# Kernel tuning notes

Measured on AMD Instinct MI355X. Metric: run time of the kernel, lower is better.

Reference implementation:

```python
import jax, jax.numpy as jnp
import numpy as np

D_MODEL = 2048
N_HEADS = 16
D_HEAD = 128
D_LATENT = 512


def setup_inputs() -> dict:
    key = jax.random.key(0)
    ks = jax.random.split(key, 5)
    s = lambda fan_in: 1.0 / np.sqrt(fan_in)
    x = jax.random.normal(ks[0], (2, 2048, D_MODEL), dtype=jnp.float32)
    # nn.Linear weights stored as [out, in]; we keep [in, out] for x @ W
    W_q = jax.random.uniform(ks[1], (D_MODEL, N_HEADS * D_HEAD), jnp.float32, -s(D_MODEL), s(D_MODEL))
    W_kv_down = jax.random.uniform(ks[2], (D_MODEL, D_LATENT), jnp.float32, -s(D_MODEL), s(D_MODEL))
    W_kv_up = jax.random.uniform(ks[3], (D_LATENT, N_HEADS * D_HEAD), jnp.float32, -s(D_LATENT), s(D_LATENT))
    W_o = jax.random.uniform(ks[4], (N_HEADS * D_HEAD, D_MODEL), jnp.float32, -s(N_HEADS * D_HEAD), s(N_HEADS * D_HEAD))
    return {"x": x, "W_q": W_q, "W_kv_down": W_kv_down, "W_kv_up": W_kv_up, "W_o": W_o}


def reference(x, W_q, W_kv_down, W_kv_up, W_o):
    B, S, _ = x.shape
    # q: [B, H, S, Dh]
    q = (x @ W_q).reshape(B, S, N_HEADS, D_HEAD).transpose(0, 2, 1, 3)
    # latent compression then up-projection; shared K = V
    latent = x @ W_kv_down                      # [B, S, Dl]
    kv = (latent @ W_kv_up).reshape(B, S, N_HEADS, D_HEAD).transpose(0, 2, 1, 3)
    scale = 1.0 / np.sqrt(D_HEAD).astype(np.float32)
    scores = jnp.einsum('bhqd,bhkd->bhqk', q, kv) * scale  # [B,H,S,S]
    probs = jax.nn.softmax(scores, axis=-1)
    out = jnp.einsum('bhqk,bhkd->bhqd', probs, kv)          # [B,H,S,Dh]
    out = out.transpose(0, 2, 1, 3).reshape(B, S, N_HEADS * D_HEAD)
    return out @ W_o
```

## Files before the change

### kernel.cpp

```cpp
#include <hip/hip_runtime.h>

typedef __attribute__((ext_vector_type(8))) __bf16 bf16x8;
typedef __attribute__((ext_vector_type(4))) float f32x4;
typedef __attribute__((ext_vector_type(8))) unsigned short u16x8;
typedef __attribute__((ext_vector_type(4))) unsigned short u16x4;

#define MFMA16(a, b, c) __builtin_amdgcn_mfma_f32_16x16x32_bf16((a), (b), (c), 0, 0, 0)

__device__ __forceinline__ unsigned short f2bf(float f) {
    unsigned int u = __float_as_uint(f);
    unsigned int r = (u + 0x7FFFu + ((u >> 16) & 1u)) >> 16;
    return (unsigned short)r;
}

__device__ __forceinline__ void transpose_tile(const float* __restrict__ in,
                                               unsigned short* __restrict__ out,
                                               int R, int C, int bx, int by) {
    __shared__ float tile[32][33];
    const int tx = threadIdx.x & 31, ty = threadIdx.x >> 5;
    const int c0 = bx * 32, r0 = by * 32;
#pragma unroll
    for (int i = 0; i < 4; ++i)
        tile[ty + i * 8][tx] = in[(size_t)(r0 + ty + i * 8) * C + c0 + tx];
    __syncthreads();
#pragma unroll
    for (int i = 0; i < 4; ++i)
        out[(size_t)(c0 + ty + i * 8) * R + r0 + tx] = f2bf(tile[tx][ty + i * 8]);
}

__global__ __launch_bounds__(256) void k_prep(const float* __restrict__ x,
                                              const float* __restrict__ Wq,
                                              const float* __restrict__ Wkvd,
                                              const float* __restrict__ Wkvu,
                                              const float* __restrict__ Wo,
                                              unsigned short* __restrict__ xb,
                                              unsigned short* __restrict__ Wcat_t,
                                              unsigned short* __restrict__ Wkvu_t,
                                              unsigned short* __restrict__ Wo_t) {
    const int i = blockIdx.x;
    if (i < 8192) {
        const int idx = i * 256 + threadIdx.x;
        const float4 v = ((const float4*)x)[idx];
        u16x4 o = { f2bf(v.x), f2bf(v.y), f2bf(v.z), f2bf(v.w) };
        ((u16x4*)xb)[idx] = o;
    } else if (i < 12288) {
        const int j = i - 8192;
        transpose_tile(Wq, Wcat_t, 2048, 2048, j & 63, j >> 6);
    } else if (i < 13312) {
        const int j = i - 12288;
        transpose_tile(Wkvd, Wcat_t + 2048 * 2048, 2048, 512, j & 15, j >> 4);
    } else if (i < 14336) {
        const int j = i - 13312;
        transpose_tile(Wkvu, Wkvu_t, 512, 2048, j & 63, j >> 6);
    } else {
        const int j = i - 14336;
        transpose_tile(Wo, Wo_t, 2048, 2048, j & 63, j >> 6);
    }
}

template <int OUT_MODE>
__global__ __launch_bounds__(256) void k_gemm_bt(const unsigned short* __restrict__ A,
                                                 const unsigned short* __restrict__ B,
                                                 void* __restrict__ Cv,
                                                 unsigned short* __restrict__ Ct,
                                                 int M, int N, int K, float alpha) {
    __shared__ alignas(16) unsigned short As[2 * 128 * 32];
    __shared__ alignas(16) unsigned short Bs[2 * 128 * 32];
    const int tid = threadIdx.x;
    const int wave = tid >> 6;
    const int lane = tid & 63;
    const int l16 = lane & 15;
    const int quad = lane >> 4;
    const int bm = blockIdx.x * 128;
    const int bn = blockIdx.y * 128;
    const int wm = (wave >> 1) * 64;
    const int wn = (wave & 1) * 64;

    const f32x4 fzero = {0.f, 0.f, 0.f, 0.f};
    f32x4 acc[4][4];
#pragma unroll
    for (int i = 0; i < 4; ++i)
#pragma unroll
        for (int j = 0; j < 4; ++j) acc[i][j] = fzero;

    auto AsL = (__attribute__((address_space(3))) unsigned short*)As;
    auto BsL = (__attribute__((address_space(3))) unsigned short*)Bs;

    const int c0 = wave * 128 + lane;

    auto stage = [&](int kt32) {
        const int boff = (kt32 & 1) * (128 * 32);
        const int kt = kt32 * 32;
#pragma unroll
        for (int j = 0; j < 2; ++j) {
            const int c = c0 + j * 64;
            __builtin_amdgcn_global_load_lds(
                (const __attribute__((address_space(1))) void*)(A + (size_t)(bm + (c >> 2)) * K + kt + (c & 3) * 8),
                (__attribute__((address_space(3))) void*)(AsL + boff + c * 8), 16, 0, 0);
            __builtin_amdgcn_global_load_lds(
                (const __attribute__((address_space(1))) void*)(B + (size_t)(bn + (c >> 2)) * K + kt + (c & 3) * 8),
                (__attribute__((address_space(3))) void*)(BsL + boff + c * 8), 16, 0, 0);
        }
    };

    const int nk = K >> 5;
    stage(0);
    for (int kt32 = 0; kt32 < nk; ++kt32) {
        __syncthreads();
        if (kt32 + 1 < nk) stage(kt32 + 1);
        const unsigned short* Ab = As + (kt32 & 1) * (128 * 32);
        const unsigned short* Bb = Bs + (kt32 & 1) * (128 * 32);

        bf16x8 af[4], bfr[4];
#pragma unroll
        for (int mt = 0; mt < 4; ++mt)
            af[mt] = *(const bf16x8*)(Ab + (wm + mt * 16 + l16) * 32 + quad * 8);
#pragma unroll
        for (int nt = 0; nt < 4; ++nt)
            bfr[nt] = *(const bf16x8*)(Bb + (wn + nt * 16 + l16) * 32 + quad * 8);
#pragma unroll
        for (int mt = 0; mt < 4; ++mt)
#pragma unroll
            for (int nt = 0; nt < 4; ++nt)
                acc[mt][nt] = MFMA16(af[mt], bfr[nt], acc[mt][nt]);
    }

#pragma unroll
    for (int mt = 0; mt < 4; ++mt)
#pragma unroll
        for (int nt = 0; nt < 4; ++nt) {
            const int row0 = bm + wm + mt * 16 + quad * 4;
            const int col = bn + wn + nt * 16 + l16;
            u16x4 pk;
#pragma unroll
            for (int r = 0; r < 4; ++r) {
                const float v0 = acc[mt][nt][r];
                if (OUT_MODE == 0) {
                    ((float*)Cv)[(size_t)(row0 + r) * N + col] = v0 * alpha;
                } else if (OUT_MODE == 3) {
                    if (col < 2048)
                        ((unsigned short*)Cv)[(size_t)(row0 + r) * 2048 + col] = f2bf(v0 * alpha);
                    else
                        Ct[(size_t)(row0 + r) * 512 + (col - 2048)] = f2bf(v0);
                } else {
                    const unsigned short b = f2bf(v0 * alpha);
                    ((unsigned short*)Cv)[(size_t)(row0 + r) * N + col] = b;
                    pk[r] = b;
                }
            }
            if (OUT_MODE == 2) {
                const size_t ti =
                    ((size_t)((row0 >> 11) * (N >> 7) + (col >> 7)) * 128 + (col & 127)) * 2048 +
                    (row0 & 2047);
                *(u16x4*)(Ct + ti) = pk;
            }
        }
}

__global__ __launch_bounds__(256, 2) void k_attn(const unsigned short* __restrict__ Q,
                                                 const unsigned short* __restrict__ KV,
                                                 const unsigned short* __restrict__ KVT,
                                                 unsigned short* __restrict__ O) {
    __shared__ alignas(16) unsigned short Ks[2 * 64 * 128];
    __shared__ alignas(16) unsigned short Vt[2 * 128 * 64];
    __shared__ alignas(16) unsigned short Ps[4 * 32 * 64];

    const int tid = threadIdx.x;
    const int wave = tid >> 6, lane = tid & 63;
    const int l16 = lane & 15, quad = lane >> 4;
    const int l8 = l16 & 7;
    const int qt = blockIdx.x;
    const int bh = blockIdx.y;
    const size_t tokbase = (size_t)(bh >> 4) * 2048;
    const int hcol = (bh & 15) * 128;
    const unsigned short* kvt_head = KVT + (size_t)bh * (128 * 2048);

    bf16x8 qf[2][4];
    const int qrow0 = qt * 128 + wave * 32;
#pragma unroll
    for (int nt = 0; nt < 2; ++nt) {
        const unsigned short* qp =
            Q + (tokbase + qrow0 + nt * 16 + l16) * 2048 + hcol + quad * 8;
#pragma unroll
        for (int kd = 0; kd < 4; ++kd) qf[nt][kd] = *(const bf16x8*)(qp + kd * 32);
    }

    const f32x4 fzero = {0.f, 0.f, 0.f, 0.f};
    f32x4 o_acc[8][2];
#pragma unroll
    for (int dt = 0; dt < 8; ++dt)
#pragma unroll
        for (int nt = 0; nt < 2; ++nt) o_acc[dt][nt] = fzero;
    float l_i[2] = {0.f, 0.f};

    const int krow = tid >> 4, kchunk = tid & 15;
    const int vrow = tid >> 3, vchunk = tid & 7;

    unsigned short* Pw = Ps + wave * (32 * 64);

    u16x8 kR[4], vR[4];
    auto load_tile = [&](int kt) {
#pragma unroll
        for (int p = 0; p < 4; ++p) {
            kR[p] = *(const u16x8*)(KV + (tokbase + kt * 64 + p * 16 + krow) * 2048 +
                                    hcol + kchunk * 8);
            vR[p] = *(const u16x8*)(kvt_head + (size_t)(p * 32 + vrow) * 2048 + kt * 64 +
                                    vchunk * 8);
        }
    };
    auto store_tile = [&](int kt) {
        unsigned short* Kb = Ks + (kt & 1) * (64 * 128);
        unsigned short* Vb = Vt + (kt & 1) * (128 * 64);
#pragma unroll
        for (int p = 0; p < 4; ++p) {
            const int r = p * 16 + krow;
            const int swk = (kchunk & 8) | ((kchunk & 7) ^ (r & 7));
            *(u16x8*)(Kb + r * 128 + swk * 8) = kR[p];
            const int d = p * 32 + vrow;
            const int swv = vchunk ^ (d & 7);
            *(u16x8*)(Vb + d * 64 + swv * 8) = vR[p];
        }
    };

    load_tile(0);
    store_tile(0);
    load_tile(1);

    for (int kt = 0; kt < 32; ++kt) {
        __syncthreads();
        if (kt < 31) {
            store_tile(kt + 1);
            if (kt < 30) load_tile(kt + 2);
        }
        const unsigned short* Kb = Ks + (kt & 1) * (64 * 128);
        const unsigned short* Vb = Vt + (kt & 1) * (128 * 64);

        f32x4 st[4][2];
#pragma unroll
        for (int mt = 0; mt < 4; ++mt)
#pragma unroll
            for (int nt = 0; nt < 2; ++nt) st[mt][nt] = fzero;
#pragma unroll
        for (int kd = 0; kd < 4; ++kd)
#pragma unroll
            for (int mt = 0; mt < 4; ++mt) {
                const int c = kd * 4 + quad;
                const int sw = (c & 8) | ((c & 7) ^ l8);
                const bf16x8 kf = *(const bf16x8*)(Kb + (mt * 16 + l16) * 128 + sw * 8);
                st[mt][0] = MFMA16(kf, qf[0][kd], st[mt][0]);
                st[mt][1] = MFMA16(kf, qf[1][kd], st[mt][1]);
            }

#pragma unroll
        for (int nt = 0; nt < 2; ++nt) {
            float rs = 0.f;
            unsigned short* prow = Pw + (nt * 16 + l16) * 64;
#pragma unroll
            for (int mt = 0; mt < 4; ++mt) {
                u16x4 pk;
#pragma unroll
                for (int r = 0; r < 4; ++r) {
                    const float p = __expf(st[mt][nt][r]);
                    rs += p;
                    pk[r] = f2bf(p);
                }
                const int c = mt * 2 + (quad >> 1);
                *(u16x4*)(prow + (c ^ l8) * 8 + (quad & 1) * 4) = pk;
            }
            rs += __shfl_xor(rs, 16);
            rs += __shfl_xor(rs, 32);
            l_i[nt] += rs;
        }

        __builtin_amdgcn_sched_barrier(0);

#pragma unroll
        for (int s = 0; s < 2; ++s) {
            const int c = s * 4 + quad;
            const int sw = (c ^ l8) * 8;
            bf16x8 pfr[2];
#pragma unroll
            for (int nt = 0; nt < 2; ++nt)
                pfr[nt] = *(const bf16x8*)(Pw + (nt * 16 + l16) * 64 + sw);
#pragma unroll
            for (int dt = 0; dt < 8; ++dt) {
                const bf16x8 vf = *(const bf16x8*)(Vb + (dt * 16 + l16) * 64 + sw);
                o_acc[dt][0] = MFMA16(vf, pfr[0], o_acc[dt][0]);
                o_acc[dt][1] = MFMA16(vf, pfr[1], o_acc[dt][1]);
            }
        }
    }

#pragma unroll
    for (int nt = 0; nt < 2; ++nt) {
        const float inv = 1.0f / l_i[nt];
        unsigned short* dst = O + (tokbase + qrow0 + nt * 16 + l16) * 2048 + hcol;
#pragma unroll
        for (int dt = 0; dt < 8; ++dt) {
            u16x4 pk;
#pragma unroll
            for (int r = 0; r < 4; ++r) pk[r] = f2bf(o_acc[dt][nt][r] * inv);
            *(u16x4*)(dst + dt * 16 + quad * 4) = pk;
        }
    }
}

extern "C" void kernel_launch(void* const* d_in, const int* in_sizes, int n_in,
                              void* d_out, int out_size, void* d_ws, size_t ws_size,
                              hipStream_t stream) {
    const float* x = (const float*)d_in[0];
    const float* W_q = (const float*)d_in[1];
    const float* W_kvd = (const float*)d_in[2];
    const float* W_kvu = (const float*)d_in[3];
    const float* W_o = (const float*)d_in[4];

    char* w = (char*)d_ws;
    unsigned short* xb = (unsigned short*)(w);
    unsigned short* kvT = xb;
    unsigned short* qb = (unsigned short*)(w + (size_t)16 * 1024 * 1024);
    unsigned short* kvb = (unsigned short*)(w + (size_t)32 * 1024 * 1024);
    unsigned short* Wo_t = (unsigned short*)(w + (size_t)48 * 1024 * 1024);
    unsigned short* Wcat_t = (unsigned short*)(w + (size_t)56 * 1024 * 1024);
    unsigned short* Wkvu_t = (unsigned short*)(w + (size_t)66 * 1024 * 1024);
    unsigned short* lat = (unsigned short*)(w + (size_t)68 * 1024 * 1024);

    k_prep<<<18432, 256, 0, stream>>>(x, W_q, W_kvd, W_kvu, W_o, xb, Wcat_t, Wkvu_t, Wo_t);

    k_gemm_bt<3><<<dim3(32, 20), 256, 0, stream>>>(xb, Wcat_t, qb, lat, 4096, 2560, 2048,
                                                   0.08838834764831845f);
    k_gemm_bt<2><<<dim3(32, 16), 256, 0, stream>>>(lat, Wkvu_t, kvb, kvT, 4096, 2048, 512,
                                                   1.0f);
    k_attn<<<dim3(16, 32), 256, 0, stream>>>(qb, kvb, kvT, qb);
    k_gemm_bt<0><<<dim3(32, 16), 256, 0, stream>>>(qb, Wo_t, d_out, nullptr, 4096, 2048, 2048,
                                                   1.0f);
}
```

Before: 320.8 us.

## Stage attention K/V via direct global-to-LDS loads and coalesce KV-transpose epilogue

The attention kernel now fills its double-buffered K and V^T tiles with global_load_lds, loading straight into LDS instead of going through registers. The LDS layout changes to a chunk-major arrangement so each wave's 16-byte chunks land contiguously without swizzling, which frees registers and removes the separate store phase. The GEMM that writes the transposed KV buffer now stages the tile in shared memory and writes it out in coalesced 16-byte rows rather than scattered 4-element stores. Risks: the prefetch depth drops to one tile issued after the barrier, with no explicit wait on the async loads before the tile is read, and the unswizzled layout may cause LDS bank conflicts.

```diff
diff --git a/kernel.cpp b/kernel.cpp
--- a/kernel.cpp
+++ b/kernel.cpp
@@ -125,44 +125,65 @@
                 acc[mt][nt] = MFMA16(af[mt], bfr[nt], acc[mt][nt]);
     }
 
-#pragma unroll
-    for (int mt = 0; mt < 4; ++mt)
-#pragma unroll
-        for (int nt = 0; nt < 4; ++nt) {
-            const int row0 = bm + wm + mt * 16 + quad * 4;
-            const int col = bn + wn + nt * 16 + l16;
-            u16x4 pk;
-#pragma unroll
-            for (int r = 0; r < 4; ++r) {
-                const float v0 = acc[mt][nt][r];
-                if (OUT_MODE == 0) {
-                    ((float*)Cv)[(size_t)(row0 + r) * N + col] = v0 * alpha;
-                } else if (OUT_MODE == 3) {
-                    if (col < 2048)
-                        ((unsigned short*)Cv)[(size_t)(row0 + r) * 2048 + col] = f2bf(v0 * alpha);
-                    else
-                        Ct[(size_t)(row0 + r) * 512 + (col - 2048)] = f2bf(v0);
-                } else {
-                    const unsigned short b = f2bf(v0 * alpha);
-                    ((unsigned short*)Cv)[(size_t)(row0 + r) * N + col] = b;
+    if constexpr (OUT_MODE == 2) {
+        __shared__ alignas(16) unsigned short Cs[128 * 136];
+#pragma unroll
+        for (int mt = 0; mt < 4; ++mt)
+#pragma unroll
+            for (int nt = 0; nt < 4; ++nt) {
+                const int row0 = wm + mt * 16 + quad * 4;
+                const int col = wn + nt * 16 + l16;
+                u16x4 pk;
+#pragma unroll
+                for (int r = 0; r < 4; ++r) {
+                    const unsigned short b = f2bf(acc[mt][nt][r] * alpha);
+                    ((unsigned short*)Cv)[(size_t)(bm + row0 + r) * N + bn + col] = b;
                     pk[r] = b;
                 }
-            }
-            if (OUT_MODE == 2) {
-                const size_t ti =
-                    ((size_t)((row0 >> 11) * (N >> 7) + (col >> 7)) * 128 + (col & 127)) * 2048 +
-                    (row0 & 2047);
-                *(u16x4*)(Ct + ti) = pk;
-            }
-        }
+                *(u16x4*)(Cs + col * 136 + row0) = pk;
+            }
+        __syncthreads();
+        unsigned short* kvt_dst =
+            Ct + ((size_t)((bm >> 11) * (N >> 7) + (bn >> 7)) * 128) * 2048 + (bm & 2047);
+#pragma unroll
+        for (int p = 0; p < 8; ++p) {
+            const int id = tid + p * 256;
+            const int d = id >> 4, sc = id & 15;
+            *(u16x8*)(kvt_dst + (size_t)d * 2048 + sc * 8) =
+                *(const u16x8*)(Cs + d * 136 + sc * 8);
+        }
+    } else {
+#pragma unroll
+        for (int mt = 0; mt < 4; ++mt)
+#pragma unroll
+            for (int nt = 0; nt < 4; ++nt) {
+                const int row0 = bm + wm + mt * 16 + quad * 4;
+                const int col = bn + wn + nt * 16 + l16;
+#pragma unroll
+                for (int r = 0; r < 4; ++r) {
+                    const float v0 = acc[mt][nt][r];
+                    if (OUT_MODE == 0) {
+                        ((float*)Cv)[(size_t)(row0 + r) * N + col] = v0 * alpha;
+                    } else if (OUT_MODE == 3) {
+                        if (col < 2048)
+                            ((unsigned short*)Cv)[(size_t)(row0 + r) * 2048 + col] =
+                                f2bf(v0 * alpha);
+                        else
+                            Ct[(size_t)(row0 + r) * 512 + (col - 2048)] = f2bf(v0);
+                    } else {
+                        ((unsigned short*)Cv)[(size_t)(row0 + r) * N + col] = f2bf(v0 * alpha);
+                    }
+                }
+            }
+    }
 }
 
 __global__ __launch_bounds__(256, 2) void k_attn(const unsigned short* __restrict__ Q,
                                                  const unsigned short* __restrict__ KV,
                                                  const unsigned short* __restrict__ KVT,
                                                  unsigned short* __restrict__ O) {
-    __shared__ alignas(16) unsigned short Ks[2 * 64 * 128];
-    __shared__ alignas(16) unsigned short Vt[2 * 128 * 64];
+    __shared__ alignas(16) unsigned short Ks[2 * 16 * 64 * 8];
+    __shared__ alignas(16) unsigned short Vt[2 * 8 * 128 * 8];
     __shared__ alignas(16) unsigned short Ps[4 * 32 * 64];
 
     const int tid = threadIdx.x;
@@ -175,6 +196,9 @@
     const int hcol = (bh & 15) * 128;
     const unsigned short* kvt_head = KVT + (size_t)bh * (128 * 2048);
 
+    auto KsL = (__attribute__((address_space(3))) unsigned short*)Ks;
+    auto VtL = (__attribute__((address_space(3))) unsigned short*)Vt;
+
     bf16x8 qf[2][4];
     const int qrow0 = qt * 128 + wave * 32;
 #pragma unroll
@@ -193,47 +217,33 @@
         for (int nt = 0; nt < 2; ++nt) o_acc[dt][nt] = fzero;
     float l_i[2] = {0.f, 0.f};
 
-    const int krow = tid >> 4, kchunk = tid & 15;
-    const int vrow = tid >> 3, vchunk = tid & 7;
-
     unsigned short* Pw = Ps + wave * (32 * 64);
 
-    u16x8 kR[4], vR[4];
-    auto load_tile = [&](int kt) {
+    auto stage = [&](int kt) {
+        const int boff = (kt & 1) * 8192;
 #pragma unroll
         for (int p = 0; p < 4; ++p) {
-            kR[p] = *(const u16x8*)(KV + (tokbase + kt * 64 + p * 16 + krow) * 2048 +
-                                    hcol + kchunk * 8);
-            vR[p] = *(const u16x8*)(kvt_head + (size_t)(p * 32 + vrow) * 2048 + kt * 64 +
-                                    vchunk * 8);
+            const int u = wave * 4 + p;
+            __builtin_amdgcn_global_load_lds(
+                (const __attribute__((address_space(1))) void*)(
+                    KV + (tokbase + kt * 64 + lane) * 2048 + hcol + u * 8),
+                (__attribute__((address_space(3))) void*)(KsL + boff + (u * 64 + lane) * 8),
+                16, 0, 0);
+            const int cv = u >> 1, d0 = (u & 1) * 64;
+            __builtin_amdgcn_global_load_lds(
+                (const __attribute__((address_space(1))) void*)(
+                    kvt_head + (size_t)(d0 + lane) * 2048 + kt * 64 + cv * 8),
+                (__attribute__((address_space(3))) void*)(VtL + boff + (cv * 128 + d0 + lane) * 8),
+                16, 0, 0);
         }
     };
-    auto store_tile = [&](int kt) {
-        unsigned short* Kb = Ks + (kt & 1) * (64 * 128);
-        unsigned short* Vb = Vt + (kt & 1) * (128 * 64);
-#pragma unroll
-        for (int p = 0; p < 4; ++p) {
-            const int r = p * 16 + krow;
-            const int swk = (kchunk & 8) | ((kchunk & 7) ^ (r & 7));
-            *(u16x8*)(Kb + r * 128 + swk * 8) = kR[p];
-            const int d = p * 32 + vrow;
-            const int swv = vchunk ^ (d & 7);
-            *(u16x8*)(Vb + d * 64 + swv * 8) = vR[p];
-        }
-    };
-
-    load_tile(0);
-    store_tile(0);
-    load_tile(1);
-
+
+    stage(0);
     for (int kt = 0; kt < 32; ++kt) {
         __syncthreads();
-        if (kt < 31) {
-            store_tile(kt + 1);
-            if (kt < 30) load_tile(kt + 2);
-        }
-        const unsigned short* Kb = Ks + (kt & 1) * (64 * 128);
-        const unsigned short* Vb = Vt + (kt & 1) * (128 * 64);
+        if (kt + 1 < 32) stage(kt + 1);
+        const unsigned short* Kb = Ks + (kt & 1) * 8192;
+        const unsigned short* Vb = Vt + (kt & 1) * 8192;
 
         f32x4 st[4][2];
 #pragma unroll
@@ -244,9 +254,8 @@
         for (int kd = 0; kd < 4; ++kd)
 #pragma unroll
             for (int mt = 0; mt < 4; ++mt) {
-                const int c = kd * 4 + quad;
-                const int sw = (c & 8) | ((c & 7) ^ l8);
-                const bf16x8 kf = *(const bf16x8*)(Kb + (mt * 16 + l16) * 128 + sw * 8);
+                const bf16x8 kf =
+                    *(const bf16x8*)(Kb + ((kd * 4 + quad) * 64 + mt * 16 + l16) * 8);
                 st[mt][0] = MFMA16(kf, qf[0][kd], st[mt][0]);
                 st[mt][1] = MFMA16(kf, qf[1][kd], st[mt][1]);
             }
@@ -276,15 +285,15 @@
 
 #pragma unroll
         for (int s = 0; s < 2; ++s) {
-            const int c = s * 4 + quad;
-            const int sw = (c ^ l8) * 8;
+            const int sw = ((s * 4 + quad) ^ l8) * 8;
             bf16x8 pfr[2];
 #pragma unroll
             for (int nt = 0; nt < 2; ++nt)
                 pfr[nt] = *(const bf16x8*)(Pw + (nt * 16 + l16) * 64 + sw);
 #pragma unroll
             for (int dt = 0; dt < 8; ++dt) {
-                const bf16x8 vf = *(const bf16x8*)(Vb + (dt * 16 + l16) * 64 + sw);
+                const bf16x8 vf =
+                    *(const bf16x8*)(Vb + ((s * 4 + quad) * 128 + dt * 16 + l16) * 8);
                 o_acc[dt][0] = MFMA16(vf, pfr[0], o_acc[dt][0]);
                 o_acc[dt][1] = MFMA16(vf, pfr[1], o_acc[dt][1]);
             }
```

Result: slower. 351.6 us (+9.6%).
